# Optimization experiments

Hardware: AMD Instinct MI355X
Metric: run time of the kernel (lower is better)

## Reference

```python
import jax, jax.numpy as jnp
import numpy as np

N = 50000
E = 800000
F_IN = 256
HID = 96
N_CLS = 32
NEG_SLOPE = 0.2


def setup_inputs() -> dict:
    key = jax.random.key(0)
    ks = jax.random.split(key, 10)
    x = jax.random.normal(ks[0], (N, F_IN), dtype=jnp.float32)
    edge_index = jax.random.randint(ks[1], (2, E), 0, N, dtype=jnp.int64)
    s1 = 1.0 / np.sqrt(F_IN)
    s2 = 1.0 / np.sqrt(HID)
    return {
        "x": x,
        "edge_index": edge_index,
        "W1": jax.random.normal(ks[2], (F_IN, HID), dtype=jnp.float32) * s1,
        "a1_src": jax.random.normal(ks[3], (HID,), dtype=jnp.float32) * s2,
        "a1_dst": jax.random.normal(ks[4], (HID,), dtype=jnp.float32) * s2,
        "b1": jnp.zeros((HID,), dtype=jnp.float32),
        "W2": jax.random.normal(ks[5], (HID, N_CLS), dtype=jnp.float32) * s2,
        "a2_src": jax.random.normal(ks[6], (N_CLS,), dtype=jnp.float32) * (1.0 / np.sqrt(N_CLS)),
        "a2_dst": jax.random.normal(ks[7], (N_CLS,), dtype=jnp.float32) * (1.0 / np.sqrt(N_CLS)),
        "b2": jnp.zeros((N_CLS,), dtype=jnp.float32),
    }


def _gat_conv(x, src, dst, W, a_src, a_dst, b, n_nodes):
    # single-head GATConv (PyG defaults), self-loops already in src/dst
    h = x @ W                                  # [N, out]
    alpha_src = h @ a_src                      # [N]
    alpha_dst = h @ a_dst                      # [N]
    e = alpha_src[src] + alpha_dst[dst]        # [E'] edge logits (msg j->i: dst groups)
    e = jnp.where(e > 0, e, NEG_SLOPE * e)     # leaky_relu
    # segment softmax over edges grouped by destination node
    m = jax.ops.segment_max(e, dst, num_segments=n_nodes)
    ex = jnp.exp(e - m[dst])
    denom = jax.ops.segment_sum(ex, dst, num_segments=n_nodes)
    alpha = ex / denom[dst]                    # [E']
    out = jax.ops.segment_sum(alpha[:, None] * h[src], dst, num_segments=n_nodes)
    return out + b


def reference(x, edge_index, W1, a1_src, a1_dst, b1, W2, a2_src, a2_dst, b2):
    loops = jnp.arange(N, dtype=edge_index.dtype)
    src = jnp.concatenate([edge_index[0], loops])
    dst = jnp.concatenate([edge_index[1], loops])
    h = _gat_conv(x, src, dst, W1, a1_src, a1_dst, b1, N)
    h = jax.nn.elu(h)
    # dropout omitted (eval mode, training=False)
    out = _gat_conv(h, src, dst, W2, a2_src, a2_dst, b2, N)
    return jax.nn.log_softmax(out, axis=1)
```

## Files before the change

### kernel.cpp

```cpp
#include <hip/hip_runtime.h>
#include <cstdint>
#include <cstddef>

#define NNODES 50000
#define NEDGES 800000
#define MEDGES (NEDGES + NNODES)
#define FIN    256
#define HID    96
#define NCLS   32
#define NEG_SLOPE 0.2f

#define NBUCK  391
#define BCAP   3072

typedef unsigned int uint32;
typedef __attribute__((ext_vector_type(8))) short short8;
typedef __attribute__((ext_vector_type(4))) float f32x4;

__device__ __forceinline__ ushort bf_round(float f) {
    uint32 u = __float_as_uint(f);
    u += 0x7FFFu + ((u >> 16) & 1u);
    return (ushort)(u >> 16);
}
__device__ __forceinline__ uint32 pack_bf16x2(float a, float b) {
    return (uint32)bf_round(a) | ((uint32)bf_round(b) << 16);
}
__device__ __forceinline__ float bf_lo(uint32 u) { return __uint_as_float(u << 16); }
__device__ __forceinline__ float bf_hi(uint32 u) { return __uint_as_float(u & 0xFFFF0000u); }
__device__ __forceinline__ float lrelu(float t) { return (t > 0.f) ? t : NEG_SLOPE * t; }
__device__ __forceinline__ float af(int i) { return __int_as_float(i); }
__device__ __forceinline__ float elu_fast(float t) { return (t > 0.f) ? t : (__expf(t) - 1.f); }


__global__ __launch_bounds__(256) void bucket1_kernel(const int* __restrict__ ei,
                                                      int* __restrict__ gcount,
                                                      int* __restrict__ staging) {
    __shared__ int hist[NBUCK];
    __shared__ int base_sh[NBUCK];
    for (int i = threadIdx.x; i < NBUCK; i += 256) hist[i] = 0;
    __syncthreads();

    int v[8], rk[8], bk[8];
    int e0 = blockIdx.x * 2048;
#pragma unroll
    for (int i = 0; i < 8; ++i) {
        int e = e0 + i * 256 + threadIdx.x;
        if (e < MEDGES) {
            int s, d;
            if (e < NEDGES) { s = ei[e]; d = ei[NEDGES + e]; }
            else            { s = e - NEDGES; d = s; }
            bk[i] = d >> 7;
            v[i]  = s | ((d & 127) << 16);
            rk[i] = atomicAdd(&hist[bk[i]], 1);
        } else bk[i] = -1;
    }
    __syncthreads();
    for (int i = threadIdx.x; i < NBUCK; i += 256) {
        int c = hist[i];
        base_sh[i] = c ? atomicAdd(&gcount[i], c) : 0;
    }
    __syncthreads();
#pragma unroll
    for (int i = 0; i < 8; ++i) {
        if (bk[i] >= 0) {
            int pos = base_sh[bk[i]] + rk[i];
            if (pos < BCAP)
                staging[(size_t)bk[i] * BCAP + pos] = v[i];
        }
    }
}

__global__ __launch_bounds__(256) void bucket2_kernel(const int* __restrict__ staging,
                                                      const int* __restrict__ gcount,
                                                      int* __restrict__ rowptr,
                                                      int* __restrict__ esrc) {
    __shared__ int dcount[128];
    __shared__ int dincl[128];
    __shared__ int dexcl[128];
    __shared__ int fillc[128];
    __shared__ int red_s[256];

    const int b = blockIdx.x;
    const int t = threadIdx.x;

    int pv = 0;
    for (int idx = t; idx < b; idx += 256) pv += gcount[idx];
    red_s[t] = pv;
    __syncthreads();
    for (int off2 = 128; off2; off2 >>= 1) {
        if (t < off2) red_s[t] += red_s[t + off2];
        __syncthreads();
    }
    const int ebase = red_s[0];
    const int cnt   = gcount[b];
    const int node0 = b << 7;
    const int* st   = staging + (size_t)b * BCAP;

    for (int i = t; i < 128; i += 256) { dcount[i] = 0; fillc[i] = 0; }
    __syncthreads();

    for (int i = t; i < cnt; i += 256)
        atomicAdd(&dcount[st[i] >> 16], 1);
    __syncthreads();

    if (t < 128) dincl[t] = dcount[t];
    __syncthreads();
    for (int off = 1; off < 128; off <<= 1) {
        int val = (t >= off && t < 128) ? dincl[t - off] : 0;
        __syncthreads();
        if (t < 128) dincl[t] += val;
        __syncthreads();
    }
    if (t < 128) {
        int excl = dincl[t] - dcount[t];
        dexcl[t] = excl;
        int node = node0 + t;
        if (node < NNODES) rowptr[node] = ebase + excl;
    }
    if (b == NBUCK - 1 && t == 0) rowptr[NNODES] = MEDGES;
    __syncthreads();

    for (int i = t; i < cnt; i += 256) {
        int v = st[i];
        int dd = v >> 16;
        int r = atomicAdd(&fillc[dd], 1);
        esrc[ebase + dexcl[dd] + r] = v & 0xFFFF;
    }
}


__global__ __launch_bounds__(256) void packw_kernel(const float* __restrict__ W1,
                                                    const float* __restrict__ W2,
                                                    ushort* __restrict__ W1p,
                                                    ushort* __restrict__ W2p) {
    int stride = gridDim.x * 256;
    for (int idx = blockIdx.x * 256 + threadIdx.x; idx < 6 * 8 * 64 * 8; idx += stride) {
        int j     = idx & 7;
        int lane  = (idx >> 3) & 63;
        int kstep = (idx >> 9) & 7;
        int ntile = idx >> 12;
        int k = kstep * 32 + ((lane >> 4) << 3) + j;
        int n = ntile * 16 + (lane & 15);
        W1p[idx] = bf_round(W1[(size_t)k * 96 + n]);
    }
    for (int idx = blockIdx.x * 256 + threadIdx.x; idx < 2 * 3 * 64 * 8; idx += stride) {
        int j     = idx & 7;
        int lane  = (idx >> 3) & 63;
        int kstep = (idx >> 9) % 3;
        int ntile = (idx >> 9) / 3;
        int k = kstep * 32 + ((lane >> 4) << 3) + j;
        int n = ntile * 16 + (lane & 15);
        W2p[idx] = bf_round(W2[(size_t)k * 32 + n]);
    }
}


__global__ __launch_bounds__(256) void gemm1_kernel(const float* __restrict__ x,
                                                    const ushort* __restrict__ W1p,
                                                    const float* __restrict__ a_src,
                                                    const float* __restrict__ a_dst,
                                                    ushort* __restrict__ h1,
                                                    float* __restrict__ as1,
                                                    float* __restrict__ ad1) {
    const int tid  = threadIdx.x;
    const int lane = tid & 63;
    const int wv   = tid >> 6;
    const int m    = lane & 15;
    const int quad = lane >> 4;
    const int node0 = blockIdx.x * 64;

    int arow = node0 + wv * 16 + m;
    if (arow >= NNODES) arow = NNODES - 1;
    const float* xr = x + (size_t)arow * FIN + quad * 8;

    const short8* Wp = (const short8*)W1p;

    f32x4 acc[6];
#pragma unroll
    for (int t = 0; t < 6; ++t) acc[t] = (f32x4){0.f, 0.f, 0.f, 0.f};

#pragma unroll
    for (int ks = 0; ks < 8; ++ks) {
        float4 v0 = *(const float4*)(xr + ks * 32);
        float4 v1 = *(const float4*)(xr + ks * 32 + 4);
        short8 a;
        a[0] = (short)bf_round(v0.x); a[1] = (short)bf_round(v0.y);
        a[2] = (short)bf_round(v0.z); a[3] = (short)bf_round(v0.w);
        a[4] = (short)bf_round(v1.x); a[5] = (short)bf_round(v1.y);
        a[6] = (short)bf_round(v1.z); a[7] = (short)bf_round(v1.w);
#pragma unroll
        for (int t = 0; t < 6; ++t) {
            short8 b = Wp[(t * 8 + ks) * 64 + lane];
            acc[t] = __builtin_amdgcn_mfma_f32_16x16x32_bf16(a, b, acc[t], 0, 0, 0);
        }
    }

    float as_reg[6], ad_reg[6];
#pragma unroll
    for (int t = 0; t < 6; ++t) {
        as_reg[t] = a_src[t * 16 + m];
        ad_reg[t] = a_dst[t * 16 + m];
    }

#pragma unroll
    for (int r = 0; r < 4; ++r) {
        int node = node0 + wv * 16 + quad * 4 + r;
        float ps = 0.f, pd = 0.f;
#pragma unroll
        for (int t = 0; t < 6; ++t) {
            ps += acc[t][r] * as_reg[t];
            pd += acc[t][r] * ad_reg[t];
        }
#pragma unroll
        for (int off = 1; off < 16; off <<= 1) {
            ps += __shfl_xor(ps, off);
            pd += __shfl_xor(pd, off);
        }
        if (node < NNODES) {
            ushort* hp = h1 + (size_t)node * 96 + m;
#pragma unroll
            for (int t = 0; t < 6; ++t) hp[t * 16] = bf_round(acc[t][r]);
            if (m == 0) { as1[node] = ps; ad1[node] = pd; }
        }
    }
}


__global__ __launch_bounds__(256) void gemm2_kernel(const uint32* __restrict__ y48,
                                                    const ushort* __restrict__ W2p,
                                                    const float* __restrict__ a_src,
                                                    const float* __restrict__ a_dst,
                                                    uint32* __restrict__ h2b,
                                                    float* __restrict__ as2,
                                                    float* __restrict__ ad2) {
    const int tid  = threadIdx.x;
    const int lane = tid & 63;
    const int wv   = tid >> 6;
    const int m    = lane & 15;
    const int quad = lane >> 4;
    const int node0 = blockIdx.x * 64;

    int arow = node0 + wv * 16 + m;
    if (arow >= NNODES) arow = NNODES - 1;
    const short8* Ar = (const short8*)(y48 + (size_t)arow * 48);
    const short8* Wp = (const short8*)W2p;

    f32x4 acc[2];
    acc[0] = (f32x4){0.f, 0.f, 0.f, 0.f};
    acc[1] = (f32x4){0.f, 0.f, 0.f, 0.f};

#pragma unroll
    for (int ks = 0; ks < 3; ++ks) {
        short8 a = Ar[ks * 4 + quad];
#pragma unroll
        for (int t = 0; t < 2; ++t) {
            short8 b = Wp[(t * 3 + ks) * 64 + lane];
            acc[t] = __builtin_amdgcn_mfma_f32_16x16x32_bf16(a, b, acc[t], 0, 0, 0);
        }
    }

    float as_reg[2], ad_reg[2];
#pragma unroll
    for (int t = 0; t < 2; ++t) {
        as_reg[t] = a_src[t * 16 + m];
        ad_reg[t] = a_dst[t * 16 + m];
    }

#pragma unroll
    for (int r = 0; r < 4; ++r) {
        int node = node0 + wv * 16 + quad * 4 + r;
        float ps = 0.f, pd = 0.f;
#pragma unroll
        for (int t = 0; t < 2; ++t) {
            ps += acc[t][r] * as_reg[t];
            pd += acc[t][r] * ad_reg[t];
        }
#pragma unroll
        for (int off = 1; off < 16; off <<= 1) {
            ps += __shfl_xor(ps, off);
            pd += __shfl_xor(pd, off);
        }
        if (node < NNODES) {
            h2b[(size_t)node * 16 + m] = pack_bf16x2(acc[0][r], acc[1][r]);
            if (m == 0) { as2[node] = ps; ad2[node] = pd; }
        }
    }
}


__global__ __launch_bounds__(256) void agg96_kernel(const ushort* __restrict__ h,
                                                    const float* __restrict__ asrc,
                                                    const float* __restrict__ adst,
                                                    const float* __restrict__ bias,
                                                    const int* __restrict__ rowptr,
                                                    const int* __restrict__ esrc,
                                                    uint32* __restrict__ out1b) {
    __shared__ int2 sa[4][2][32];
    const int wave = threadIdx.x >> 6;
    const int lane = threadIdx.x & 63;
    const int hf   = lane >> 5;
    const int fl32 = lane & 31;
    const int i = blockIdx.x * 8 + wave * 2 + hf;

    const int start = rowptr[i];
    const int deg   = rowptr[i + 1] - start;
    const float ad  = adst[i];
    const int fl    = (fl32 < 24) ? fl32 : 23;

    float acc0 = 0.f, acc1 = 0.f, acc2 = 0.f, acc3 = 0.f;

    if (deg <= 32) {
        bool valid = fl32 < deg;
        int s_reg = valid ? esrc[start + fl32] : 0;
        float e = valid ? lrelu(asrc[s_reg] + ad) : -1e30f;
        float mx = e;
#pragma unroll
        for (int off = 16; off; off >>= 1) mx = fmaxf(mx, __shfl_xor(mx, off));
        float ex = valid ? __expf(e - mx) : 0.f;
        float sum = ex;
#pragma unroll
        for (int off = 16; off; off >>= 1) sum += __shfl_xor(sum, off);
        sa[wave][hf][fl32] = make_int2(s_reg, __float_as_int(ex / sum));

        const int4* sap = (const int4*)&sa[wave][hf][0];

        for (int eb = 0; eb < deg; eb += 8) {
            int4 qa = sap[(eb >> 1) + 0];
            int4 qb = sap[(eb >> 1) + 1];
            int4 qc = sap[(eb >> 1) + 2];
            int4 qd = sap[(eb >> 1) + 3];
            const uint2* r0 = (const uint2*)(h + (size_t)qa.x * 96);
            const uint2* r1 = (const uint2*)(h + (size_t)qa.z * 96);
            const uint2* r2 = (const uint2*)(h + (size_t)qb.x * 96);
            const uint2* r3 = (const uint2*)(h + (size_t)qb.z * 96);
            const uint2* r4 = (const uint2*)(h + (size_t)qc.x * 96);
            const uint2* r5 = (const uint2*)(h + (size_t)qc.z * 96);
            const uint2* r6 = (const uint2*)(h + (size_t)qd.x * 96);
            const uint2* r7 = (const uint2*)(h + (size_t)qd.z * 96);
            uint2 u0 = r0[fl], u1 = r1[fl], u2 = r2[fl], u3 = r3[fl];
            uint2 u4 = r4[fl], u5 = r5[fl], u6 = r6[fl], u7 = r7[fl];
            float a0 = af(qa.y), a1 = af(qa.w), a2 = af(qb.y), a3 = af(qb.w);
            float a4 = af(qc.y), a5 = af(qc.w), a6 = af(qd.y), a7 = af(qd.w);
            acc0 += a0 * bf_lo(u0.x) + a1 * bf_lo(u1.x) + a2 * bf_lo(u2.x) + a3 * bf_lo(u3.x)
                  + a4 * bf_lo(u4.x) + a5 * bf_lo(u5.x) + a6 * bf_lo(u6.x) + a7 * bf_lo(u7.x);
            acc1 += a0 * bf_hi(u0.x) + a1 * bf_hi(u1.x) + a2 * bf_hi(u2.x) + a3 * bf_hi(u3.x)
                  + a4 * bf_hi(u4.x) + a5 * bf_hi(u5.x) + a6 * bf_hi(u6.x) + a7 * bf_hi(u7.x);
            acc2 += a0 * bf_lo(u0.y) + a1 * bf_lo(u1.y) + a2 * bf_lo(u2.y) + a3 * bf_lo(u3.y)
                  + a4 * bf_lo(u4.y) + a5 * bf_lo(u5.y) + a6 * bf_lo(u6.y) + a7 * bf_lo(u7.y);
            acc3 += a0 * bf_hi(u0.y) + a1 * bf_hi(u1.y) + a2 * bf_hi(u2.y) + a3 * bf_hi(u3.y)
                  + a4 * bf_hi(u4.y) + a5 * bf_hi(u5.y) + a6 * bf_hi(u6.y) + a7 * bf_hi(u7.y);
        }
    } else {
        float mx = -1e30f;
        for (int p = start + fl32; p < start + deg; p += 32)
            mx = fmaxf(mx, lrelu(asrc[esrc[p]] + ad));
#pragma unroll
        for (int off = 16; off; off >>= 1) mx = fmaxf(mx, __shfl_xor(mx, off));
        float sum = 0.f;
        for (int p = start + fl32; p < start + deg; p += 32)
            sum += __expf(lrelu(asrc[esrc[p]] + ad) - mx);
#pragma unroll
        for (int off = 16; off; off >>= 1) sum += __shfl_xor(sum, off);
        float inv = 1.f / sum;
        for (int e = 0; e < deg; ++e) {
            int s = esrc[start + e];
            float a = __expf(lrelu(asrc[s] + ad) - mx) * inv;
            uint2 u = ((const uint2*)(h + (size_t)s * 96))[fl];
            acc0 += a * bf_lo(u.x);
            acc1 += a * bf_hi(u.x);
            acc2 += a * bf_lo(u.y);
            acc3 += a * bf_hi(u.y);
        }
    }

    if (fl32 < 24) {
        float v0 = elu_fast(acc0 + bias[4 * fl32 + 0]);
        float v1 = elu_fast(acc1 + bias[4 * fl32 + 1]);
        float v2 = elu_fast(acc2 + bias[4 * fl32 + 2]);
        float v3 = elu_fast(acc3 + bias[4 * fl32 + 3]);
        uint2 o;
        o.x = pack_bf16x2(v0, v1);
        o.y = pack_bf16x2(v2, v3);
        *(uint2*)(out1b + (size_t)i * 48 + 2 * fl32) = o;
    }
}


__global__ __launch_bounds__(256) void agg32_kernel(const uint32* __restrict__ h2b,
                                                    const float* __restrict__ asrc,
                                                    const float* __restrict__ adst,
                                                    const float* __restrict__ bias,
                                                    const int* __restrict__ rowptr,
                                                    const int* __restrict__ esrc,
                                                    float* __restrict__ out) {
    __shared__ int2 sa[4][64];
    int wave = threadIdx.x >> 6;
    int lane = threadIdx.x & 63;
    int i = blockIdx.x * 4 + wave;
    if (i >= NNODES) return;

    int start = rowptr[i], end = rowptr[i + 1];
    int deg = end - start;
    float ad = adst[i];

    if (deg <= 64) {
        int p = start + lane;
        bool valid = p < end;
        int s_reg = valid ? esrc[p] : 0;
        float e = valid ? lrelu(asrc[s_reg] + ad) : -1e30f;
        float mx = e;
#pragma unroll
        for (int off = 32; off; off >>= 1) mx = fmaxf(mx, __shfl_xor(mx, off));
        float ex = valid ? __expf(e - mx) : 0.f;
        float sum = ex;
#pragma unroll
        for (int off = 32; off; off >>= 1) sum += __shfl_xor(sum, off);
        sa[wave][lane] = make_int2(s_reg, __float_as_int(ex / sum));

        const int g  = lane >> 3;
        const int fl = lane & 7;
        float acc[4];
#pragma unroll
        for (int j = 0; j < 4; ++j) acc[j] = 0.f;

#pragma unroll 2
        for (int eb = 0; eb < deg; eb += 8) {
            int e0 = eb + g;
            int2 qq = sa[wave][(e0 < 64) ? e0 : 63];
            float a = (e0 < deg) ? af(qq.y) : 0.f;
            const uint2* hr = (const uint2*)(h2b + (size_t)qq.x * 16);
            uint2 u = hr[fl];
            acc[0] = fmaf(a, bf_lo(u.x), acc[0]);
            acc[1] = fmaf(a, bf_hi(u.x), acc[1]);
            acc[2] = fmaf(a, bf_lo(u.y), acc[2]);
            acc[3] = fmaf(a, bf_hi(u.y), acc[3]);
        }
#pragma unroll
        for (int j = 0; j < 4; ++j) {
            acc[j] += __shfl_xor(acc[j], 8);
            acc[j] += __shfl_xor(acc[j], 16);
            acc[j] += __shfl_xor(acc[j], 32);
        }

        float z0 = acc[0] + bias[2 * fl];
        float z1 = acc[1] + bias[2 * fl + 16];
        float z2 = acc[2] + bias[2 * fl + 1];
        float z3 = acc[3] + bias[2 * fl + 17];
        float m2 = fmaxf(fmaxf(z0, z1), fmaxf(z2, z3));
#pragma unroll
        for (int off = 4; off; off >>= 1) m2 = fmaxf(m2, __shfl_xor(m2, off));
        float s2 = __expf(z0 - m2) + __expf(z1 - m2) + __expf(z2 - m2) + __expf(z3 - m2);
#pragma unroll
        for (int off = 4; off; off >>= 1) s2 += __shfl_xor(s2, off);
        float ls = m2 + __logf(s2);
        if (lane < 8) {
            float* op = out + (size_t)i * 32;
            op[2 * fl]      = z0 - ls;
            op[2 * fl + 16] = z1 - ls;
            op[2 * fl + 1]  = z2 - ls;
            op[2 * fl + 17] = z3 - ls;
        }
    } else {
        int e2 = lane >> 5;
        int f  = lane & 31;
        float mx = -1e30f;
        for (int p = start + lane; p < end; p += 64)
            mx = fmaxf(mx, lrelu(asrc[esrc[p]] + ad));
#pragma unroll
        for (int off = 32; off; off >>= 1) mx = fmaxf(mx, __shfl_xor(mx, off));
        float sum = 0.f;
        for (int p = start + lane; p < end; p += 64)
            sum += __expf(lrelu(asrc[esrc[p]] + ad) - mx);
#pragma unroll
        for (int off = 32; off; off >>= 1) sum += __shfl_xor(sum, off);
        float inv = 1.f / sum;
        float acc = 0.f;
        for (int p = start + e2; p < end; p += 2) {
            int s = esrc[p];
            float a = __expf(lrelu(asrc[s] + ad) - mx) * inv;
            uint32 u = h2b[(size_t)s * 16 + (f & 15)];
            acc += a * ((f < 16) ? bf_lo(u) : bf_hi(u));
        }
        acc += __shfl_xor(acc, 32);

        float z = acc + bias[f];
        float m2 = z;
#pragma unroll
        for (int off = 16; off; off >>= 1) m2 = fmaxf(m2, __shfl_xor(m2, off));
        float ex2 = __expf(z - m2);
        float s2 = ex2;
#pragma unroll
        for (int off = 16; off; off >>= 1) s2 += __shfl_xor(s2, off);
        if (lane < 32) out[(size_t)i * 32 + f] = z - m2 - __logf(s2);
    }
}


extern "C" void kernel_launch(void* const* d_in, const int* in_sizes, int n_in,
                              void* d_out, int out_size, void* d_ws, size_t ws_size,
                              hipStream_t stream) {
    const float* x   = (const float*)d_in[0];
    const int*   ei  = (const int*)d_in[1];
    const float* W1  = (const float*)d_in[2];
    const float* a1s = (const float*)d_in[3];
    const float* a1d = (const float*)d_in[4];
    const float* b1  = (const float*)d_in[5];
    const float* W2  = (const float*)d_in[6];
    const float* a2s = (const float*)d_in[7];
    const float* a2d = (const float*)d_in[8];
    const float* b2  = (const float*)d_in[9];
    float* out = (float*)d_out;

    size_t off = 0;
    auto alloc = [&](size_t bytes) {
        void* p = (char*)d_ws + off;
        off += (bytes + 255) & ~(size_t)255;
        return p;
    };
    ushort* h1    = (ushort*)alloc((size_t)NNODES * HID * 2);
    uint32* out1b = (uint32*)alloc((size_t)NNODES * 48 * 4);
    int*  staging = (int*)alloc((size_t)NBUCK * BCAP * 4);
    float* as1    = (float*)alloc((size_t)NNODES * 4);
    float* ad1    = (float*)alloc((size_t)NNODES * 4);
    float* as2    = (float*)alloc((size_t)NNODES * 4);
    float* ad2    = (float*)alloc((size_t)NNODES * 4);
    int*   rowptr = (int*)alloc((size_t)(NNODES + 1) * 4);
    int*   esrc   = (int*)alloc((size_t)MEDGES * 4);
    ushort* W1p   = (ushort*)alloc((size_t)6 * 8 * 64 * 8 * 2);
    ushort* W2p   = (ushort*)alloc((size_t)2 * 3 * 64 * 8 * 2);
    int*   gcount = (int*)alloc((size_t)NBUCK * 4);
    uint32* h2b   = (uint32*)h1;

    hipMemsetAsync(gcount, 0, (size_t)NBUCK * 4, stream);

    const int nbB1    = (MEDGES + 2047) / 2048;
    const int nbGemm  = (NNODES + 63) / 64;
    const int nbAgg96 = NNODES / 8;
    const int nbAgg32 = (NNODES + 3) / 4;

    packw_kernel<<<13, 256, 0, stream>>>(W1, W2, W1p, W2p);
    bucket1_kernel<<<nbB1, 256, 0, stream>>>(ei, gcount, staging);
    bucket2_kernel<<<NBUCK, 256, 0, stream>>>(staging, gcount, rowptr, esrc);

    gemm1_kernel<<<nbGemm, 256, 0, stream>>>(x, W1p, a1s, a1d, h1, as1, ad1);
    agg96_kernel<<<nbAgg96, 256, 0, stream>>>(h1, as1, ad1, b1, rowptr, esrc, out1b);

    gemm2_kernel<<<nbGemm, 256, 0, stream>>>(out1b, W2p, a2s, a2d, h2b, as2, ad2);
    agg32_kernel<<<nbAgg32, 256, 0, stream>>>(h2b, as2, ad2, b2, rowptr, esrc, out);
}
```

Before: 215.1 us.

## Process two nodes per wave in agg32 and fold gcount memset into packw

The layer-2 aggregation kernel now assigns a half-wave of 32 lanes to each destination node instead of a full wave. The fast path covers degrees up to 32, and the high-degree path shares one unified reduction and log-softmax epilogue. This raises lane utilisation, since most nodes have about 17 edges and left half of each 64-lane wave idle. More nodes now take the slower general path. Separately, the gcount zeroing moves from a hipMemsetAsync call into packw_kernel, which removes one API call.

```diff
diff --git a/kernel.cpp b/kernel.cpp
--- a/kernel.cpp
+++ b/kernel.cpp
@@ -132,8 +132,11 @@
 __global__ __launch_bounds__(256) void packw_kernel(const float* __restrict__ W1,
                                                     const float* __restrict__ W2,
                                                     ushort* __restrict__ W1p,
-                                                    ushort* __restrict__ W2p) {
+                                                    ushort* __restrict__ W2p,
+                                                    int* __restrict__ gcount) {
     int stride = gridDim.x * 256;
+    for (int idx = blockIdx.x * 256 + threadIdx.x; idx < NBUCK; idx += stride)
+        gcount[idx] = 0;
     for (int idx = blockIdx.x * 256 + threadIdx.x; idx < 6 * 8 * 64 * 8; idx += stride) {
         int j     = idx & 7;
         int lane  = (idx >> 3) & 63;
@@ -393,105 +396,95 @@
                                                     const int* __restrict__ rowptr,
                                                     const int* __restrict__ esrc,
                                                     float* __restrict__ out) {
-    __shared__ int2 sa[4][64];
-    int wave = threadIdx.x >> 6;
-    int lane = threadIdx.x & 63;
-    int i = blockIdx.x * 4 + wave;
-    if (i >= NNODES) return;
-
-    int start = rowptr[i], end = rowptr[i + 1];
-    int deg = end - start;
-    float ad = adst[i];
-
-    if (deg <= 64) {
-        int p = start + lane;
-        bool valid = p < end;
-        int s_reg = valid ? esrc[p] : 0;
+    __shared__ int2 sa[4][2][32];
+    const int wave = threadIdx.x >> 6;
+    const int lane = threadIdx.x & 63;
+    const int hf   = lane >> 5;
+    const int fl32 = lane & 31;
+    const int i = blockIdx.x * 8 + wave * 2 + hf;
+
+    const int start = rowptr[i];
+    const int deg   = rowptr[i + 1] - start;
+    const float ad  = adst[i];
+    const int g  = fl32 >> 3;
+    const int fl = fl32 & 7;
+
+    float acc[4];
+#pragma unroll
+    for (int j = 0; j < 4; ++j) acc[j] = 0.f;
+
+    if (deg <= 32) {
+        bool valid = fl32 < deg;
+        int s_reg = valid ? esrc[start + fl32] : 0;
         float e = valid ? lrelu(asrc[s_reg] + ad) : -1e30f;
         float mx = e;
 #pragma unroll
-        for (int off = 32; off; off >>= 1) mx = fmaxf(mx, __shfl_xor(mx, off));
+        for (int off = 16; off; off >>= 1) mx = fmaxf(mx, __shfl_xor(mx, off));
         float ex = valid ? __expf(e - mx) : 0.f;
         float sum = ex;
 #pragma unroll
-        for (int off = 32; off; off >>= 1) sum += __shfl_xor(sum, off);
-        sa[wave][lane] = make_int2(s_reg, __float_as_int(ex / sum));
-
-        const int g  = lane >> 3;
-        const int fl = lane & 7;
-        float acc[4];
-#pragma unroll
-        for (int j = 0; j < 4; ++j) acc[j] = 0.f;
+        for (int off = 16; off; off >>= 1) sum += __shfl_xor(sum, off);
+        sa[wave][hf][fl32] = make_int2(s_reg, __float_as_int(ex / sum));
 
 #pragma unroll 2
-        for (int eb = 0; eb < deg; eb += 8) {
+        for (int eb = 0; eb < deg; eb += 4) {
             int e0 = eb + g;
-            int2 qq = sa[wave][(e0 < 64) ? e0 : 63];
-            float a = (e0 < deg) ? af(qq.y) : 0.f;
-            const uint2* hr = (const uint2*)(h2b + (size_t)qq.x * 16);
+            int2 q = sa[wave][hf][(e0 < 32) ? e0 : 31];
+            float a = (e0 < deg) ? af(q.y) : 0.f;
+            const uint2* hr = (const uint2*)(h2b + (size_t)q.x * 16);
             uint2 u = hr[fl];
             acc[0] = fmaf(a, bf_lo(u.x), acc[0]);
             acc[1] = fmaf(a, bf_hi(u.x), acc[1]);
             acc[2] = fmaf(a, bf_lo(u.y), acc[2]);
             acc[3] = fmaf(a, bf_hi(u.y), acc[3]);
         }
-#pragma unroll
-        for (int j = 0; j < 4; ++j) {
-            acc[j] += __shfl_xor(acc[j], 8);
-            acc[j] += __shfl_xor(acc[j], 16);
-            acc[j] += __shfl_xor(acc[j], 32);
-        }
-
-        float z0 = acc[0] + bias[2 * fl];
-        float z1 = acc[1] + bias[2 * fl + 16];
-        float z2 = acc[2] + bias[2 * fl + 1];
-        float z3 = acc[3] + bias[2 * fl + 17];
-        float m2 = fmaxf(fmaxf(z0, z1), fmaxf(z2, z3));
-#pragma unroll
-        for (int off = 4; off; off >>= 1) m2 = fmaxf(m2, __shfl_xor(m2, off));
-        float s2 = __expf(z0 - m2) + __expf(z1 - m2) + __expf(z2 - m2) + __expf(z3 - m2);
-#pragma unroll
-        for (int off = 4; off; off >>= 1) s2 += __shfl_xor(s2, off);
-        float ls = m2 + __logf(s2);
-        if (lane < 8) {
-            float* op = out + (size_t)i * 32;
-            op[2 * fl]      = z0 - ls;
-            op[2 * fl + 16] = z1 - ls;
-            op[2 * fl + 1]  = z2 - ls;
-            op[2 * fl + 17] = z3 - ls;
-        }
     } else {
-        int e2 = lane >> 5;
-        int f  = lane & 31;
         float mx = -1e30f;
-        for (int p = start + lane; p < end; p += 64)
+        for (int p = start + fl32; p < start + deg; p += 32)
             mx = fmaxf(mx, lrelu(asrc[esrc[p]] + ad));
 #pragma unroll
-        for (int off = 32; off; off >>= 1) mx = fmaxf(mx, __shfl_xor(mx, off));
+        for (int off = 16; off; off >>= 1) mx = fmaxf(mx, __shfl_xor(mx, off));
         float sum = 0.f;
-        for (int p = start + lane; p < end; p += 64)
+        for (int p = start + fl32; p < start + deg; p += 32)
             sum += __expf(lrelu(asrc[esrc[p]] + ad) - mx);
 #pragma unroll
-        for (int off = 32; off; off >>= 1) sum += __shfl_xor(sum, off);
+        for (int off = 16; off; off >>= 1) sum += __shfl_xor(sum, off);
         float inv = 1.f / sum;
-        float acc = 0.f;
-        for (int p = start + e2; p < end; p += 2) {
+        for (int p = start + g; p < start + deg; p += 4) {
             int s = esrc[p];
             float a = __expf(lrelu(asrc[s] + ad) - mx) * inv;
-            uint32 u = h2b[(size_t)s * 16 + (f & 15)];
-            acc += a * ((f < 16) ? bf_lo(u) : bf_hi(u));
-        }
-        acc += __shfl_xor(acc, 32);
-
-        float z = acc + bias[f];
-        float m2 = z;
-#pragma unroll
-        for (int off = 16; off; off >>= 1) m2 = fmaxf(m2, __shfl_xor(m2, off));
-        float ex2 = __expf(z - m2);
-        float s2 = ex2;
-#pragma unroll
-        for (int off = 16; off; off >>= 1) s2 += __shfl_xor(s2, off);
-        if (lane < 32) out[(size_t)i * 32 + f] = z - m2 - __logf(s2);
+            const uint2* hr = (const uint2*)(h2b + (size_t)s * 16);
+            uint2 u = hr[fl];
+            acc[0] = fmaf(a, bf_lo(u.x), acc[0]);
+            acc[1] = fmaf(a, bf_hi(u.x), acc[1]);
+            acc[2] = fmaf(a, bf_lo(u.y), acc[2]);
+            acc[3] = fmaf(a, bf_hi(u.y), acc[3]);
+        }
+    }
+
+#pragma unroll
+    for (int j = 0; j < 4; ++j) {
+        acc[j] += __shfl_xor(acc[j], 8);
+        acc[j] += __shfl_xor(acc[j], 16);
+    }
+
+    float z0 = acc[0] + bias[2 * fl];
+    float z1 = acc[1] + bias[2 * fl + 16];
+    float z2 = acc[2] + bias[2 * fl + 1];
+    float z3 = acc[3] + bias[2 * fl + 17];
+    float m2 = fmaxf(fmaxf(z0, z1), fmaxf(z2, z3));
+#pragma unroll
+    for (int off = 4; off; off >>= 1) m2 = fmaxf(m2, __shfl_xor(m2, off));
+    float s2 = __expf(z0 - m2) + __expf(z1 - m2) + __expf(z2 - m2) + __expf(z3 - m2);
+#pragma unroll
+    for (int off = 4; off; off >>= 1) s2 += __shfl_xor(s2, off);
+    float ls = m2 + __logf(s2);
+    if (fl32 < 8) {
+        float* op = out + (size_t)i * 32;
+        op[2 * fl]      = z0 - ls;
+        op[2 * fl + 16] = z1 - ls;
+        op[2 * fl + 1]  = z2 - ls;
+        op[2 * fl + 17] = z3 - ls;
     }
 }
 
@@ -531,20 +524,17 @@
     int*   gcount = (int*)alloc((size_t)NBUCK * 4);
     uint32* h2b   = (uint32*)h1;
 
-    hipMemsetAsync(gcount, 0, (size_t)NBUCK * 4, stream);
-
     const int nbB1    = (MEDGES + 2047) / 2048;
     const int nbGemm  = (NNODES + 63) / 64;
-    const int nbAgg96 = NNODES / 8;
-    const int nbAgg32 = (NNODES + 3) / 4;
-
-    packw_kernel<<<13, 256, 0, stream>>>(W1, W2, W1p, W2p);
+    const int nbAggP  = NNODES / 8;
+
+    packw_kernel<<<13, 256, 0, stream>>>(W1, W2, W1p, W2p, gcount);
     bucket1_kernel<<<nbB1, 256, 0, stream>>>(ei, gcount, staging);
     bucket2_kernel<<<NBUCK, 256, 0, stream>>>(staging, gcount, rowptr, esrc);
 
     gemm1_kernel<<<nbGemm, 256, 0, stream>>>(x, W1p, a1s, a1d, h1, as1, ad1);
-    agg96_kernel<<<nbAgg96, 256, 0, stream>>>(h1, as1, ad1, b1, rowptr, esrc, out1b);
+    agg96_kernel<<<nbAggP, 256, 0, stream>>>(h1, as1, ad1, b1, rowptr, esrc, out1b);
 
     gemm2_kernel<<<nbGemm, 256, 0, stream>>>(out1b, W2p, a2s, a2d, h2b, as2, ad2);
-    agg32_kernel<<<nbAgg32, 256, 0, stream>>>(h2b, as2, ad2, b2, rowptr, esrc, out);
-}
+    agg32_kernel<<<nbAggP, 256, 0, stream>>>(h2b, as2, ad2, b2, rowptr, esrc, out);
+}
```

Result: faster. 205.1 us (-4.6%).
